# Optimization experiments

Measured on AMD Instinct MI355X. Metric: run time of the kernel, lower is better.

Reference implementation:

```python
import jax, jax.numpy as jnp
import numpy as np

N = 50000      # nodes
E = 800000     # edges (avg degree 16)
IN = 128       # in_channels
OUT = 64       # out_channels
HID = 2 * OUT  # 128, hidden width of conv1
EPS = 1e-5     # BatchNorm eps


def _edge_norm(edge_index):
    # PyG ChebConv with sym normalization, lambda_max=2: L_hat = -D^{-1/2} A D^{-1/2}
    src, dst = edge_index[0], edge_index[1]
    deg = jax.ops.segment_sum(jnp.ones((E,), jnp.float32), src, num_segments=N)
    dinv = jnp.where(deg > 0, jax.lax.rsqrt(jnp.maximum(deg, 1.0)), 0.0)
    return -dinv[src] * dinv[dst]


def _cheb(x, src, dst, norm, W0, W1, b):
    # K=2 Chebyshev conv: Tx0 = x, Tx1 = L_hat x (sparse propagate)
    tx1 = jax.ops.segment_sum(x[src] * norm[:, None], dst, num_segments=N)
    return x @ W0 + tx1 @ W1 + b


def setup_inputs() -> dict:
    key = jax.random.key(0)
    ks = jax.random.split(key, 14)
    g = lambda k, shp, fan: jax.random.normal(k, shp, jnp.float32) / np.sqrt(fan)
    return {
        "x": jax.random.normal(ks[0], (N, IN), jnp.float32),
        "edge_index": jax.random.randint(ks[1], (2, E), 0, N, dtype=jnp.int32),
        "W1_0": g(ks[2], (IN, HID), IN),
        "W1_1": g(ks[3], (IN, HID), IN),
        "b1": jnp.zeros((HID,), jnp.float32),
        "gamma": jnp.ones((HID,), jnp.float32),
        "beta": jnp.zeros((HID,), jnp.float32),
        "Wmu_0": g(ks[4], (HID, OUT), HID),
        "Wmu_1": g(ks[5], (HID, OUT), HID),
        "b_mu": jnp.zeros((OUT,), jnp.float32),
        "Wls_0": g(ks[6], (HID, OUT), HID),
        "Wls_1": g(ks[7], (HID, OUT), HID),
        "b_ls": jnp.zeros((OUT,), jnp.float32),
    }


def reference(x, edge_index, W1_0, W1_1, b1, gamma, beta,
              Wmu_0, Wmu_1, b_mu, Wls_0, Wls_1, b_ls):
    src, dst = edge_index[0], edge_index[1]
    norm = _edge_norm(edge_index)
    h = _cheb(x, src, dst, norm, W1_0, W1_1, b1)         # [N, HID]
    # BatchNorm1d (training mode: batch statistics over nodes)
    mean = jnp.mean(h, axis=0)
    var = jnp.var(h, axis=0)
    h = (h - mean) * jax.lax.rsqrt(var + EPS) * gamma + beta
    h = jax.nn.relu(h)
    mu = _cheb(h, src, dst, norm, Wmu_0, Wmu_1, b_mu)    # [N, OUT]
    logstd = _cheb(h, src, dst, norm, Wls_0, Wls_1, b_ls)
    return (mu, logstd)
```

## Files before the change

### kernel.cpp

```cpp
#include <hip/hip_runtime.h>
#include <cstddef>
#include <cstdint>

static constexpr int IN_C  = 128;
static constexpr float BN_EPS = 1e-5f;
static constexpr int OUT_C = 64;

static constexpr int CS_C = 32;
static constexpr int NMAX = 50000;
static constexpr int NHALF = NMAX / 2;

using bf16x8 = __attribute__((ext_vector_type(8))) short;
using f32x4  = __attribute__((ext_vector_type(4))) float;

__device__ __forceinline__ ushort f2bf(float f) {
    uint u = __float_as_uint(f);
    u += 0x7fffu + ((u >> 16) & 1u);
    return (ushort)(u >> 16);
}
__device__ __forceinline__ uint pack2(float a, float b) {
    return (uint)f2bf(a) | ((uint)f2bf(b) << 16);
}
__device__ __forceinline__ float bf_lo(uint v) { return __uint_as_float(v << 16); }
__device__ __forceinline__ float bf_hi(uint v) { return __uint_as_float(v & 0xffff0000u); }

__device__ __forceinline__ int swz8(int row, int g) { return (g ^ ((row >> 1) & 3)) * 8; }

__global__ __launch_bounds__(1024) void hist_conv_k(
    const int* __restrict__ src, const int* __restrict__ dst,
    ushort* __restrict__ hsrc_part, ushort* __restrict__ hdst_part,
    int N, int E, int chunk, int nb_x,
    const float* __restrict__ x, ushort* __restrict__ xb,
    const float* __restrict__ W1_0, const float* __restrict__ W1_1,
    const float* __restrict__ b1,
    const float* __restrict__ Wmu_0, const float* __restrict__ Wmu_1,
    const float* __restrict__ b_mu,
    const float* __restrict__ Wls_0, const float* __restrict__ Wls_1,
    const float* __restrict__ b_ls,
    ushort* __restrict__ Wt1, ushort* __restrict__ Wt2,
    float* __restrict__ bias1, float* __restrict__ bias2) {
    __shared__ uint hp[NHALF];
    int bid = blockIdx.x;
    int tid = threadIdx.x;
    if (bid < 2 * CS_C) {
        bool is_dst = (bid >= CS_C);
        int c = is_dst ? bid - CS_C : bid;
        const int* ea = is_dst ? dst : src;
        ushort* outp = is_dst ? hdst_part : hsrc_part;
        for (int j = tid; j < NHALF; j += 1024) hp[j] = 0u;
        __syncthreads();
        int e0 = c * chunk, e1 = min(e0 + chunk, E);
        for (int i = e0 + tid; i < e1; i += 1024) {
            int s = ea[i];
            atomicAdd(&hp[s >> 1], 1u << ((s & 1) * 16));
        }
        __syncthreads();
        uint* op = (uint*)(outp + (size_t)c * N);
        for (int j = tid; j < N / 2; j += 1024) op[j] = hp[j];
    } else if (bid < 2 * CS_C + nb_x) {
        int i = (bid - 2 * CS_C) * 1024 + tid;
        if (i < N * 64) {
            float2 v = ((const float2*)x)[i];
            ((uint*)xb)[i] = pack2(v.x, v.y);
        }
    } else {
        int idx = (bid - 2 * CS_C - nb_x) * 1024 + tid;
        int which = idx >> 15;
        int c = (idx >> 8) & 127;
        int k = idx & 255;
        if (which == 0) {
            float v = (k < 128) ? W1_0[k * 128 + c] : W1_1[(k - 128) * 128 + c];
            Wt1[c * 256 + k] = f2bf(v);
            if (k == 0) bias1[c] = b1[c];
        } else {
            float v;
            if (c < 64) v = (k < 128) ? Wmu_0[k * 64 + c] : Wmu_1[(k - 128) * 64 + c];
            else        v = (k < 128) ? Wls_0[k * 64 + (c - 64)] : Wls_1[(k - 128) * 64 + (c - 64)];
            Wt2[c * 256 + k] = f2bf(v);
            if (k == 0) bias2[c] = (c < 64) ? b_mu[c] : b_ls[c - 64];
        }
    }
}

__global__ __launch_bounds__(256) void count_k(
    const ushort* __restrict__ hsrc_part, const ushort* __restrict__ hdst_part,
    float* __restrict__ dinv, int* __restrict__ cnt_dst,
    int* __restrict__ bsum, float* __restrict__ stats, int N) {
    __shared__ int sw[4];
    int tid = threadIdx.x;
    if (blockIdx.x == 0) stats[tid] = 0.f;
    int v = blockIdx.x * 256 + tid;
    int b = 0;
    if (v < N) {
        int a = 0;
        for (int c = 0; c < CS_C; ++c) {
            a += hsrc_part[(size_t)c * N + v];
            b += hdst_part[(size_t)c * N + v];
        }
        dinv[v] = (a > 0) ? rsqrtf((float)a) : 0.f;
        cnt_dst[v] = b;
    }
    int t = b;
    #pragma unroll
    for (int off = 1; off < 64; off <<= 1) t += __shfl_xor(t, off, 64);
    if ((tid & 63) == 0) sw[tid >> 6] = t;
    __syncthreads();
    if (tid == 0) bsum[blockIdx.x] = sw[0] + sw[1] + sw[2] + sw[3];
}

__global__ __launch_bounds__(256) void phase3_k(
    const int* __restrict__ cnt, const int* __restrict__ bsum,
    int* __restrict__ row_ptr, const ushort* __restrict__ hdst_part,
    int* __restrict__ offs, int n, int nb) {
    __shared__ int sbp[4];
    __shared__ int swv[4];
    int tid = threadIdx.x;
    int lane = tid & 63, wave = tid >> 6;
    int bv = (tid < nb && tid < (int)blockIdx.x) ? bsum[tid] : 0;
    int t = bv;
    #pragma unroll
    for (int off = 1; off < 64; off <<= 1) t += __shfl_xor(t, off, 64);
    if (lane == 0) sbp[wave] = t;
    int v = blockIdx.x * 256 + tid;
    int c = (v < n) ? cnt[v] : 0;
    int s = c;
    #pragma unroll
    for (int off = 1; off < 64; off <<= 1) {
        int u = __shfl_up(s, off, 64);
        if (lane >= off) s += u;
    }
    if (lane == 63) swv[wave] = s;
    __syncthreads();
    int bpre = sbp[0] + sbp[1] + sbp[2] + sbp[3];
    int wexcl = 0;
    for (int w = 0; w < wave; ++w) wexcl += swv[w];
    int st = bpre + wexcl + (s - c);
    if (v < n) row_ptr[v + 1] = st + c;
    if (v == 0) row_ptr[0] = 0;
    int r = st;
    for (int ch = 0; ch < CS_C; ++ch) {
        size_t idx = (size_t)ch * n + v;
        if (v < n) {
            offs[idx] = r;
            r += hdst_part[idx];
        }
    }
}

__global__ __launch_bounds__(1024) void scatter_k(
    const int* __restrict__ src, const int* __restrict__ dst,
    const int* __restrict__ offs, ushort* __restrict__ col,
    int N, int E, int chunk) {
    __shared__ uint dp[NHALF];
    int tid = threadIdx.x;
    int c = blockIdx.x;
    for (int j = tid; j < NHALF; j += 1024) dp[j] = 0u;
    __syncthreads();
    const int* offc = offs + (size_t)c * N;
    int e0 = c * chunk, e1 = min(e0 + chunk, E);
    for (int i = e0 + tid; i < e1; i += 1024) {
        int t = dst[i];
        int s = src[i];
        uint d = atomicAdd(&dp[t >> 1], 1u << ((t & 1) * 16));
        uint delta = (d >> ((t & 1) * 16)) & 0xffffu;
        int pos = offc[t] + (int)delta;
        col[pos] = (ushort)s;
    }
}

#define FMA8(V, D)                                                            \
  { float v0_ = bf_lo((V).x), v1_ = bf_hi((V).x), v2_ = bf_lo((V).y),         \
          v3_ = bf_hi((V).y), v4_ = bf_lo((V).z), v5_ = bf_hi((V).z),         \
          v6_ = bf_lo((V).w), v7_ = bf_hi((V).w);                             \
    if (BN) {                                                                 \
      v0_ = fmaxf(v0_ * sc[0] + sh[0], 0.f);                                  \
      v1_ = fmaxf(v1_ * sc[1] + sh[1], 0.f);                                  \
      v2_ = fmaxf(v2_ * sc[2] + sh[2], 0.f);                                  \
      v3_ = fmaxf(v3_ * sc[3] + sh[3], 0.f);                                  \
      v4_ = fmaxf(v4_ * sc[4] + sh[4], 0.f);                                  \
      v5_ = fmaxf(v5_ * sc[5] + sh[5], 0.f);                                  \
      v6_ = fmaxf(v6_ * sc[6] + sh[6], 0.f);                                  \
      v7_ = fmaxf(v7_ * sc[7] + sh[7], 0.f);                                  \
    }                                                                         \
    acc[0] += v0_ * (D); acc[1] += v1_ * (D); acc[2] += v2_ * (D);            \
    acc[3] += v3_ * (D); acc[4] += v4_ * (D); acc[5] += v5_ * (D);            \
    acc[6] += v6_ * (D); acc[7] += v7_ * (D); }

template <int BN>
__global__ __launch_bounds__(256) void propagate4_k(
    const uint4* __restrict__ xs, uint4* __restrict__ out,
    const int* __restrict__ row_ptr, const ushort* __restrict__ colu,
    const float* __restrict__ dinv, int n,
    const float* __restrict__ stats, const float* __restrict__ gamma,
    const float* __restrict__ beta, float inv_n) {
    int wid = (blockIdx.x * 256 + threadIdx.x) >> 6;
    if (wid >= n) return;
    int lane = threadIdx.x & 63;
    int g = lane >> 4, li = lane & 15;
    float sc[8], sh[8];
    if (BN) {
        #pragma unroll
        for (int j = 0; j < 8; ++j) {
            int f = li * 8 + j;
            float mean = stats[f] * inv_n;
            float var = stats[128 + f] * inv_n - mean * mean;
            float s = gamma[f] * rsqrtf(var + BN_EPS);
            sc[j] = s;
            sh[j] = beta[f] - mean * s;
        }
    }
    int s = row_ptr[wid], e = row_ptr[wid + 1];
    float acc[8];
    #pragma unroll
    for (int k = 0; k < 8; ++k) acc[k] = 0.f;
    int i = s + g;
    for (; i + 12 < e; i += 16) {
        int c0 = (int)colu[i];
        int c1 = (int)colu[i + 4];
        int c2 = (int)colu[i + 8];
        int c3 = (int)colu[i + 12];
        float d0 = dinv[c0], d1 = dinv[c1], d2 = dinv[c2], d3 = dinv[c3];
        uint4 v0 = xs[(size_t)c0 * 16 + li];
        uint4 v1 = xs[(size_t)c1 * 16 + li];
        uint4 v2 = xs[(size_t)c2 * 16 + li];
        uint4 v3 = xs[(size_t)c3 * 16 + li];
        FMA8(v0, d0); FMA8(v1, d1); FMA8(v2, d2); FMA8(v3, d3);
    }
    for (; i < e; i += 4) {
        int c0 = (int)colu[i];
        float d0 = dinv[c0];
        uint4 v0 = xs[(size_t)c0 * 16 + li];
        FMA8(v0, d0);
    }
    #pragma unroll
    for (int k = 0; k < 8; ++k) {
        acc[k] += __shfl_xor(acc[k], 16, 64);
        acc[k] += __shfl_xor(acc[k], 32, 64);
    }
    if (g == 0) {
        float scl = -dinv[wid];
        uint4 o;
        o.x = pack2(acc[0] * scl, acc[1] * scl);
        o.y = pack2(acc[2] * scl, acc[3] * scl);
        o.z = pack2(acc[4] * scl, acc[5] * scl);
        o.w = pack2(acc[6] * scl, acc[7] * scl);
        out[(size_t)wid * 16 + li] = o;
    }
}

template <int MODE>
__global__ __launch_bounds__(256) void gemm_mfma_k(
    const ushort* __restrict__ A0, const ushort* __restrict__ A1,
    const ushort* __restrict__ Wt, const float* __restrict__ bias,
    ushort* __restrict__ Cb, float* __restrict__ Cmu, float* __restrict__ Cls,
    float* __restrict__ stats, int n,
    const float* __restrict__ gamma, const float* __restrict__ beta,
    float inv_n) {
    __shared__ ushort sA[64][32];
    __shared__ ushort sW[128][32];
    __shared__ float smS[4][128];
    __shared__ float smQ[4][128];
    __shared__ float sp[256];

    int tid = threadIdx.x;
    int block_row = blockIdx.x * 64;
    int wave = tid >> 6, lane = tid & 63;
    int col_base = lane & 15;
    int quad = lane >> 4;
    int m_local = wave * 16 + col_base;

    if (MODE == 1) {
        if (tid < 128) {
            float mean = stats[tid] * inv_n;
            float var = stats[128 + tid] * inv_n - mean * mean;
            float s = gamma[tid] * rsqrtf(var + BN_EPS);
            sp[tid] = s;
            sp[128 + tid] = beta[tid] - mean * s;
        }
        __syncthreads();
    }

    f32x4 acc[8];
    #pragma unroll
    for (int t = 0; t < 8; ++t) acc[t] = (f32x4){0.f, 0.f, 0.f, 0.f};

    for (int k0 = 0; k0 < 256; k0 += 32) {
        {
            int row = tid >> 2, g = tid & 3;
            int grow = block_row + row;
            int kc = k0 + g * 8;
            uint4 v = make_uint4(0, 0, 0, 0);
            if (grow < n) {
                const ushort* srcp = (kc < 128) ? (A0 + (size_t)grow * 128 + kc)
                                                : (A1 + (size_t)grow * 128 + (kc - 128));
                v = *(const uint4*)srcp;
                if (MODE == 1 && kc < 128) {
                    float a0 = fmaxf(bf_lo(v.x) * sp[kc + 0] + sp[128 + kc + 0], 0.f);
                    float a1 = fmaxf(bf_hi(v.x) * sp[kc + 1] + sp[128 + kc + 1], 0.f);
                    float a2 = fmaxf(bf_lo(v.y) * sp[kc + 2] + sp[128 + kc + 2], 0.f);
                    float a3 = fmaxf(bf_hi(v.y) * sp[kc + 3] + sp[128 + kc + 3], 0.f);
                    float a4 = fmaxf(bf_lo(v.z) * sp[kc + 4] + sp[128 + kc + 4], 0.f);
                    float a5 = fmaxf(bf_hi(v.z) * sp[kc + 5] + sp[128 + kc + 5], 0.f);
                    float a6 = fmaxf(bf_lo(v.w) * sp[kc + 6] + sp[128 + kc + 6], 0.f);
                    float a7 = fmaxf(bf_hi(v.w) * sp[kc + 7] + sp[128 + kc + 7], 0.f);
                    v.x = pack2(a0, a1); v.y = pack2(a2, a3);
                    v.z = pack2(a4, a5); v.w = pack2(a6, a7);
                }
            }
            *(uint4*)&sA[row][swz8(row, g)] = v;
        }
        #pragma unroll
        for (int i = tid; i < 512; i += 256) {
            int c = i >> 2, g = i & 3;
            *(uint4*)&sW[c][swz8(c, g)] = *(const uint4*)(Wt + (size_t)c * 256 + k0 + g * 8);
        }
        __syncthreads();
        bf16x8 af = *(const bf16x8*)&sA[m_local][swz8(m_local, quad)];
        #pragma unroll
        for (int t = 0; t < 8; ++t) {
            int wr = t * 16 + col_base;
            bf16x8 bfr = *(const bf16x8*)&sW[wr][swz8(wr, quad)];
            acc[t] = __builtin_amdgcn_mfma_f32_16x16x32_bf16(af, bfr, acc[t], 0, 0, 0);
        }
        __syncthreads();
    }

    int row_l = wave * 16 + quad * 4;
    #pragma unroll
    for (int t = 0; t < 8; ++t) {
        int col = t * 16 + col_base;
        float b = bias[col];
        float s = 0.f, q = 0.f;
        #pragma unroll
        for (int r = 0; r < 4; ++r) {
            int grow = block_row + row_l + r;
            if (grow < n) {
                float v = acc[t][r] + b;
                if (MODE == 0) {
                    Cb[(size_t)grow * 128 + col] = f2bf(v);
                    s += v; q += v * v;
                } else {
                    if (col < 64) Cmu[(size_t)grow * 64 + col] = v;
                    else          Cls[(size_t)grow * 64 + (col - 64)] = v;
                }
            }
        }
        if (MODE == 0) {
            s += __shfl_xor(s, 16, 64); s += __shfl_xor(s, 32, 64);
            q += __shfl_xor(q, 16, 64); q += __shfl_xor(q, 32, 64);
            if (quad == 0) { smS[wave][col] = s; smQ[wave][col] = q; }
        }
    }
    if (MODE == 0) {
        __syncthreads();
        if (tid < 128) {
            float s = smS[0][tid] + smS[1][tid] + smS[2][tid] + smS[3][tid];
            float q = smQ[0][tid] + smQ[1][tid] + smQ[2][tid] + smQ[3][tid];
            atomicAdd(&stats[tid], s);
            atomicAdd(&stats[128 + tid], q);
        }
    }
}

extern "C" void kernel_launch(void* const* d_in, const int* in_sizes, int n_in,
                              void* d_out, int out_size, void* d_ws, size_t ws_size,
                              hipStream_t stream) {
    const float* x = (const float*)d_in[0];
    const int* edge_index = (const int*)d_in[1];
    const float* W1_0 = (const float*)d_in[2];
    const float* W1_1 = (const float*)d_in[3];
    const float* b1 = (const float*)d_in[4];
    const float* gamma = (const float*)d_in[5];
    const float* beta = (const float*)d_in[6];
    const float* Wmu_0 = (const float*)d_in[7];
    const float* Wmu_1 = (const float*)d_in[8];
    const float* b_mu = (const float*)d_in[9];
    const float* Wls_0 = (const float*)d_in[10];
    const float* Wls_1 = (const float*)d_in[11];
    const float* b_ls = (const float*)d_in[12];

    const int N = in_sizes[0] / IN_C;
    const int E = in_sizes[1] / 2;
    const int* src = edge_index;
    const int* dst = edge_index + E;

    char* w = (char*)d_ws;
    auto alloc = [&](size_t bytes) {
        char* p = w;
        w += (bytes + 15) & ~(size_t)15;
        return p;
    };
    float* stats = (float*)alloc(256 * 4);
    int* row_ptr = (int*)alloc((size_t)(N + 1) * 4);
    int* bsum    = (int*)alloc(256 * 4);
    float* dinv  = (float*)alloc((size_t)N * 4);
    int* cnt_dst = (int*)alloc((size_t)N * 4);
    ushort* col  = (ushort*)alloc((size_t)E * 2);
    ushort* hsrc_part = (ushort*)alloc((size_t)CS_C * N * 2);
    ushort* hdst_part = (ushort*)alloc((size_t)CS_C * N * 2);
    int* offs    = (int*)alloc((size_t)CS_C * N * 4);
    ushort* x_bf  = (ushort*)alloc((size_t)N * 128 * 2);
    ushort* xp_bf = (ushort*)alloc((size_t)N * 128 * 2);
    ushort* h_bf  = (ushort*)alloc((size_t)N * 128 * 2);
    ushort* Wt1   = (ushort*)alloc(128 * 256 * 2);
    ushort* Wt2   = (ushort*)alloc(128 * 256 * 2);
    float* bias1  = (float*)alloc(128 * 4);
    float* bias2  = (float*)alloc(128 * 4);

    float* out_mu = (float*)d_out;
    float* out_ls = out_mu + (size_t)N * OUT_C;

    int chunk = (E + CS_C - 1) / CS_C;
    int NBLK = (N + 255) / 256;
    int nb_x = (N * 64 + 1023) / 1024;
    int nb_w = 64;
    float inv_n = 1.f / (float)N;

    hist_conv_k<<<2 * CS_C + nb_x + nb_w, 1024, 0, stream>>>(
        src, dst, hsrc_part, hdst_part, N, E, chunk, nb_x,
        x, x_bf, W1_0, W1_1, b1, Wmu_0, Wmu_1, b_mu, Wls_0, Wls_1, b_ls,
        Wt1, Wt2, bias1, bias2);
    count_k<<<NBLK, 256, 0, stream>>>(hsrc_part, hdst_part, dinv, cnt_dst, bsum, stats, N);
    phase3_k<<<NBLK, 256, 0, stream>>>(cnt_dst, bsum, row_ptr, hdst_part, offs, N, NBLK);
    scatter_k<<<CS_C, 1024, 0, stream>>>(src, dst, offs, col, N, E, chunk);

    int pb = (N + 3) / 4;
    propagate4_k<0><<<pb, 256, 0, stream>>>((const uint4*)x_bf, (uint4*)xp_bf,
                                            row_ptr, col, dinv, N,
                                            nullptr, nullptr, nullptr, 0.f);

    int gb = (N + 63) / 64;
    gemm_mfma_k<0><<<gb, 256, 0, stream>>>(x_bf, xp_bf, Wt1, bias1, h_bf,
                                           nullptr, nullptr, stats, N,
                                           nullptr, nullptr, 0.f);

    propagate4_k<1><<<pb, 256, 0, stream>>>((const uint4*)h_bf, (uint4*)xp_bf,
                                            row_ptr, col, dinv, N,
                                            stats, gamma, beta, inv_n);

    gemm_mfma_k<1><<<gb, 256, 0, stream>>>(h_bf, xp_bf, Wt2, bias2, nullptr,
                                           out_mu, out_ls, stats, N,
                                           gamma, beta, inv_n);
}
```

Before: 304.0 us.

## Fuse sparse propagate into MFMA GEMM and range-partition CSR scatter

Each GEMM block now gathers its 64 rows' neighbour aggregates directly into LDS before the MFMA loop. This removes the separate propagate kernels and the global round trip of the propagated bf16 matrix. The scatter kernel is split across node ranges, so each block keeps 6250 int cursors in LDS seeded from precomputed offsets, replacing the packed 16-bit counter trick. In exchange, every scatter block rereads its whole edge chunk, and the fused kernel has fewer, heavier blocks (782), with each wave walking 16 nodes serially, which lowers gather parallelism and latency hiding.

```diff
diff --git a/kernel.cpp b/kernel.cpp
--- a/kernel.cpp
+++ b/kernel.cpp
@@ -7,6 +7,8 @@
 static constexpr int OUT_C = 64;
 
 static constexpr int CS_C = 32;
+static constexpr int CS_R = 8;
+static constexpr int CS_RANGE = 6250;
 static constexpr int NMAX = 50000;
 static constexpr int NHALF = NMAX / 2;
 
@@ -149,22 +151,24 @@
 
 __global__ __launch_bounds__(1024) void scatter_k(
     const int* __restrict__ src, const int* __restrict__ dst,
-    const int* __restrict__ offs, ushort* __restrict__ col,
-    int N, int E, int chunk) {
-    __shared__ uint dp[NHALF];
-    int tid = threadIdx.x;
-    int c = blockIdx.x;
-    for (int j = tid; j < NHALF; j += 1024) dp[j] = 0u;
+    const int* __restrict__ off, ushort* __restrict__ col,
+    int N, int E, int chunk, int range) {
+    __shared__ int cur[CS_RANGE];
+    int c = blockIdx.x & (CS_C - 1);
+    int r = blockIdx.x / CS_C;
+    int base = r * range;
+    int hi = min(base + range, N);
+    int rsz = hi - base;
+    for (int j = threadIdx.x; j < rsz; j += 1024)
+        cur[j] = off[(size_t)c * N + base + j];
     __syncthreads();
-    const int* offc = offs + (size_t)c * N;
     int e0 = c * chunk, e1 = min(e0 + chunk, E);
-    for (int i = e0 + tid; i < e1; i += 1024) {
+    for (int i = e0 + threadIdx.x; i < e1; i += 1024) {
         int t = dst[i];
-        int s = src[i];
-        uint d = atomicAdd(&dp[t >> 1], 1u << ((t & 1) * 16));
-        uint delta = (d >> ((t & 1) * 16)) & 0xffffu;
-        int pos = offc[t] + (int)delta;
-        col[pos] = (ushort)s;
+        if (t >= base && t < hi) {
+            int pos = atomicAdd(&cur[t - base], 1);
+            col[pos] = (ushort)src[i];
+        }
     }
 }
 
@@ -172,7 +176,7 @@
   { float v0_ = bf_lo((V).x), v1_ = bf_hi((V).x), v2_ = bf_lo((V).y),         \
           v3_ = bf_hi((V).y), v4_ = bf_lo((V).z), v5_ = bf_hi((V).z),         \
           v6_ = bf_lo((V).w), v7_ = bf_hi((V).w);                             \
-    if (BN) {                                                                 \
+    if (MODE == 1) {                                                          \
       v0_ = fmaxf(v0_ * sc[0] + sh[0], 0.f);                                  \
       v1_ = fmaxf(v1_ * sc[1] + sh[1], 0.f);                                  \
       v2_ = fmaxf(v2_ * sc[2] + sh[2], 0.f);                                  \
@@ -186,71 +190,12 @@
     acc[3] += v3_ * (D); acc[4] += v4_ * (D); acc[5] += v5_ * (D);            \
     acc[6] += v6_ * (D); acc[7] += v7_ * (D); }
 
-template <int BN>
-__global__ __launch_bounds__(256) void propagate4_k(
-    const uint4* __restrict__ xs, uint4* __restrict__ out,
+template <int MODE>
+__global__ __launch_bounds__(256) void fused_pg_k(
+    const uint4* __restrict__ xsg,
+    const ushort* __restrict__ A0,
     const int* __restrict__ row_ptr, const ushort* __restrict__ colu,
-    const float* __restrict__ dinv, int n,
-    const float* __restrict__ stats, const float* __restrict__ gamma,
-    const float* __restrict__ beta, float inv_n) {
-    int wid = (blockIdx.x * 256 + threadIdx.x) >> 6;
-    if (wid >= n) return;
-    int lane = threadIdx.x & 63;
-    int g = lane >> 4, li = lane & 15;
-    float sc[8], sh[8];
-    if (BN) {
-        #pragma unroll
-        for (int j = 0; j < 8; ++j) {
-            int f = li * 8 + j;
-            float mean = stats[f] * inv_n;
-            float var = stats[128 + f] * inv_n - mean * mean;
-            float s = gamma[f] * rsqrtf(var + BN_EPS);
-            sc[j] = s;
-            sh[j] = beta[f] - mean * s;
-        }
-    }
-    int s = row_ptr[wid], e = row_ptr[wid + 1];
-    float acc[8];
-    #pragma unroll
-    for (int k = 0; k < 8; ++k) acc[k] = 0.f;
-    int i = s + g;
-    for (; i + 12 < e; i += 16) {
-        int c0 = (int)colu[i];
-        int c1 = (int)colu[i + 4];
-        int c2 = (int)colu[i + 8];
-        int c3 = (int)colu[i + 12];
-        float d0 = dinv[c0], d1 = dinv[c1], d2 = dinv[c2], d3 = dinv[c3];
-        uint4 v0 = xs[(size_t)c0 * 16 + li];
-        uint4 v1 = xs[(size_t)c1 * 16 + li];
-        uint4 v2 = xs[(size_t)c2 * 16 + li];
-        uint4 v3 = xs[(size_t)c3 * 16 + li];
-        FMA8(v0, d0); FMA8(v1, d1); FMA8(v2, d2); FMA8(v3, d3);
-    }
-    for (; i < e; i += 4) {
-        int c0 = (int)colu[i];
-        float d0 = dinv[c0];
-        uint4 v0 = xs[(size_t)c0 * 16 + li];
-        FMA8(v0, d0);
-    }
-    #pragma unroll
-    for (int k = 0; k < 8; ++k) {
-        acc[k] += __shfl_xor(acc[k], 16, 64);
-        acc[k] += __shfl_xor(acc[k], 32, 64);
-    }
-    if (g == 0) {
-        float scl = -dinv[wid];
-        uint4 o;
-        o.x = pack2(acc[0] * scl, acc[1] * scl);
-        o.y = pack2(acc[2] * scl, acc[3] * scl);
-        o.z = pack2(acc[4] * scl, acc[5] * scl);
-        o.w = pack2(acc[6] * scl, acc[7] * scl);
-        out[(size_t)wid * 16 + li] = o;
-    }
-}
-
-template <int MODE>
-__global__ __launch_bounds__(256) void gemm_mfma_k(
-    const ushort* __restrict__ A0, const ushort* __restrict__ A1,
+    const float* __restrict__ dinv,
     const ushort* __restrict__ Wt, const float* __restrict__ bias,
     ushort* __restrict__ Cb, float* __restrict__ Cmu, float* __restrict__ Cls,
     float* __restrict__ stats, int n,
@@ -258,6 +203,7 @@
     float inv_n) {
     __shared__ ushort sA[64][32];
     __shared__ ushort sW[128][32];
+    __shared__ ushort xpL[64][136];
     __shared__ float smS[4][128];
     __shared__ float smQ[4][128];
     __shared__ float sp[256];
@@ -265,9 +211,6 @@
     int tid = threadIdx.x;
     int block_row = blockIdx.x * 64;
     int wave = tid >> 6, lane = tid & 63;
-    int col_base = lane & 15;
-    int quad = lane >> 4;
-    int m_local = wave * 16 + col_base;
 
     if (MODE == 1) {
         if (tid < 128) {
@@ -280,6 +223,68 @@
         __syncthreads();
     }
 
+    {
+        int g = lane >> 4, li = lane & 15;
+        float sc[8], sh[8];
+        if (MODE == 1) {
+            #pragma unroll
+            for (int j = 0; j < 8; ++j) {
+                sc[j] = sp[li * 8 + j];
+                sh[j] = sp[128 + li * 8 + j];
+            }
+        }
+        for (int t = 0; t < 16; ++t) {
+            int ndl = wave * 16 + t;
+            int nd = block_row + ndl;
+            float acc[8];
+            #pragma unroll
+            for (int k = 0; k < 8; ++k) acc[k] = 0.f;
+            float scl = 0.f;
+            if (nd < n) {
+                scl = -dinv[nd];
+                int s = row_ptr[nd], e = row_ptr[nd + 1];
+                int i = s + g;
+                for (; i + 12 < e; i += 16) {
+                    int c0 = (int)colu[i];
+                    int c1 = (int)colu[i + 4];
+                    int c2 = (int)colu[i + 8];
+                    int c3 = (int)colu[i + 12];
+                    float d0 = dinv[c0], d1 = dinv[c1];
+                    float d2 = dinv[c2], d3 = dinv[c3];
+                    uint4 v0 = xsg[(size_t)c0 * 16 + li];
+                    uint4 v1 = xsg[(size_t)c1 * 16 + li];
+                    uint4 v2 = xsg[(size_t)c2 * 16 + li];
+                    uint4 v3 = xsg[(size_t)c3 * 16 + li];
+                    FMA8(v0, d0); FMA8(v1, d1); FMA8(v2, d2); FMA8(v3, d3);
+                }
+                for (; i < e; i += 4) {
+                    int c0 = (int)colu[i];
+                    float d0 = dinv[c0];
+                    uint4 v0 = xsg[(size_t)c0 * 16 + li];
+                    FMA8(v0, d0);
+                }
+            }
+            #pragma unroll
+            for (int k = 0; k < 8; ++k) {
+                acc[k] += __shfl_xor(acc[k], 16, 64);
+                acc[k] += __shfl_xor(acc[k], 32, 64);
+            }
+            if (g == 0) {
+                uint4 o;
+                o.x = pack2(acc[0] * scl, acc[1] * scl);
+                o.y = pack2(acc[2] * scl, acc[3] * scl);
+                o.z = pack2(acc[4] * scl, acc[5] * scl);
+                o.w = pack2(acc[6] * scl, acc[7] * scl);
+                *(uint4*)&xpL[ndl][li * 8] = o;
+            }
+        }
+    }
+    __syncthreads();
+
+    int col_base = lane & 15;
+    int quad = lane >> 4;
+    int m_local = wave * 16 + col_base;
+
     f32x4 acc[8];
     #pragma unroll
     for (int t = 0; t < 8; ++t) acc[t] = (f32x4){0.f, 0.f, 0.f, 0.f};
@@ -290,22 +295,24 @@
             int grow = block_row + row;
             int kc = k0 + g * 8;
             uint4 v = make_uint4(0, 0, 0, 0);
-            if (grow < n) {
-                const ushort* srcp = (kc < 128) ? (A0 + (size_t)grow * 128 + kc)
-                                                : (A1 + (size_t)grow * 128 + (kc - 128));
-                v = *(const uint4*)srcp;
-                if (MODE == 1 && kc < 128) {
-                    float a0 = fmaxf(bf_lo(v.x) * sp[kc + 0] + sp[128 + kc + 0], 0.f);
-                    float a1 = fmaxf(bf_hi(v.x) * sp[kc + 1] + sp[128 + kc + 1], 0.f);
-                    float a2 = fmaxf(bf_lo(v.y) * sp[kc + 2] + sp[128 + kc + 2], 0.f);
-                    float a3 = fmaxf(bf_hi(v.y) * sp[kc + 3] + sp[128 + kc + 3], 0.f);
-                    float a4 = fmaxf(bf_lo(v.z) * sp[kc + 4] + sp[128 + kc + 4], 0.f);
-                    float a5 = fmaxf(bf_hi(v.z) * sp[kc + 5] + sp[128 + kc + 5], 0.f);
-                    float a6 = fmaxf(bf_lo(v.w) * sp[kc + 6] + sp[128 + kc + 6], 0.f);
-                    float a7 = fmaxf(bf_hi(v.w) * sp[kc + 7] + sp[128 + kc + 7], 0.f);
-                    v.x = pack2(a0, a1); v.y = pack2(a2, a3);
-                    v.z = pack2(a4, a5); v.w = pack2(a6, a7);
+            if (kc < 128) {
+                if (grow < n) {
+                    v = *(const uint4*)(A0 + (size_t)grow * 128 + kc);
+                    if (MODE == 1) {
+                        float a0 = fmaxf(bf_lo(v.x) * sp[kc + 0] + sp[128 + kc + 0], 0.f);
+                        float a1 = fmaxf(bf_hi(v.x) * sp[kc + 1] + sp[128 + kc + 1], 0.f);
+                        float a2 = fmaxf(bf_lo(v.y) * sp[kc + 2] + sp[128 + kc + 2], 0.f);
+                        float a3 = fmaxf(bf_hi(v.y) * sp[kc + 3] + sp[128 + kc + 3], 0.f);
+                        float a4 = fmaxf(bf_lo(v.z) * sp[kc + 4] + sp[128 + kc + 4], 0.f);
+                        float a5 = fmaxf(bf_hi(v.z) * sp[kc + 5] + sp[128 + kc + 5], 0.f);
+                        float a6 = fmaxf(bf_lo(v.w) * sp[kc + 6] + sp[128 + kc + 6], 0.f);
+                        float a7 = fmaxf(bf_hi(v.w) * sp[kc + 7] + sp[128 + kc + 7], 0.f);
+                        v.x = pack2(a0, a1); v.y = pack2(a2, a3);
+                        v.z = pack2(a4, a5); v.w = pack2(a6, a7);
+                    }
                 }
+            } else {
+                v = *(const uint4*)&xpL[row][kc - 128];
             }
             *(uint4*)&sA[row][swz8(row, g)] = v;
         }
@@ -400,7 +407,6 @@
     ushort* hdst_part = (ushort*)alloc((size_t)CS_C * N * 2);
     int* offs    = (int*)alloc((size_t)CS_C * N * 4);
     ushort* x_bf  = (ushort*)alloc((size_t)N * 128 * 2);
-    ushort* xp_bf = (ushort*)alloc((size_t)N * 128 * 2);
     ushort* h_bf  = (ushort*)alloc((size_t)N * 128 * 2);
     ushort* Wt1   = (ushort*)alloc(128 * 256 * 2);
     ushort* Wt2   = (ushort*)alloc(128 * 256 * 2);
@@ -411,6 +417,7 @@
     float* out_ls = out_mu + (size_t)N * OUT_C;
 
     int chunk = (E + CS_C - 1) / CS_C;
+    int range = (N + CS_R - 1) / CS_R;
     int NBLK = (N + 255) / 256;
     int nb_x = (N * 64 + 1023) / 1024;
     int nb_w = 64;
@@ -422,23 +429,14 @@
         Wt1, Wt2, bias1, bias2);
     count_k<<<NBLK, 256, 0, stream>>>(hsrc_part, hdst_part, dinv, cnt_dst, bsum, stats, N);
     phase3_k<<<NBLK, 256, 0, stream>>>(cnt_dst, bsum, row_ptr, hdst_part, offs, N, NBLK);
-    scatter_k<<<CS_C, 1024, 0, stream>>>(src, dst, offs, col, N, E, chunk);
-
-    int pb = (N + 3) / 4;
-    propagate4_k<0><<<pb, 256, 0, stream>>>((const uint4*)x_bf, (uint4*)xp_bf,
-                                            row_ptr, col, dinv, N,
-                                            nullptr, nullptr, nullptr, 0.f);
+    scatter_k<<<CS_R * CS_C, 1024, 0, stream>>>(src, dst, offs, col, N, E, chunk, range);
 
     int gb = (N + 63) / 64;
-    gemm_mfma_k<0><<<gb, 256, 0, stream>>>(x_bf, xp_bf, Wt1, bias1, h_bf,
-                                           nullptr, nullptr, stats, N,
-                                           nullptr, nullptr, 0.f);
-
-    propagate4_k<1><<<pb, 256, 0, stream>>>((const uint4*)h_bf, (uint4*)xp_bf,
-                                            row_ptr, col, dinv, N,
-                                            stats, gamma, beta, inv_n);
-
-    gemm_mfma_k<1><<<gb, 256, 0, stream>>>(h_bf, xp_bf, Wt2, bias2, nullptr,
-                                           out_mu, out_ls, stats, N,
-                                           gamma, beta, inv_n);
-}
+    fused_pg_k<0><<<gb, 256, 0, stream>>>(
+        (const uint4*)x_bf, x_bf, row_ptr, col, dinv, Wt1, bias1,
+        h_bf, nullptr, nullptr, stats, N, nullptr, nullptr, 0.f);
+
+    fused_pg_k<1><<<gb, 256, 0, stream>>>(
+        (const uint4*)h_bf, h_bf, row_ptr, col, dinv, Wt2, bias2,
+        nullptr, out_mu, out_ls, stats, N, gamma, beta, inv_n);
+}
```

Result: faster. 278.9 us (-8.3%).
